# Kernel optimization log

Hardware: AMD Instinct MI355X
Metric: run time of the kernel (lower is better)

Reference implementation:

```python
import jax, jax.numpy as jnp
import numpy as np

N, L, H, D = 4, 2048, 16, 32   # batch, seq len, heads, projection_dim
DIM = H * D                     # 512 model dim


def setup_inputs() -> dict:
    rng = jax.random.key(0)
    k1, k2, k3, k4, k5 = jax.random.split(rng, 5)
    query = jax.random.normal(k1, (N, L, DIM), dtype=jnp.float32)
    key = jax.random.normal(k2, (N, L, DIM), dtype=jnp.float32)
    scale = 0.02
    Wq = jax.random.normal(k3, (DIM, DIM), dtype=jnp.float32) * scale
    Wk = jax.random.normal(k4, (DIM, DIM), dtype=jnp.float32) * scale
    Wv = jax.random.normal(k5, (DIM, DIM), dtype=jnp.float32) * scale
    return {"query": query, "key": key, "Wq": Wq, "Wk": Wk, "Wv": Wv, "mask": 1}


def reference(query, key, Wq, Wk, Wv, mask):
    # torch Linear(bias=False): y = x @ W^T
    n, Lq, _ = query.shape
    _, Lk, _ = key.shape
    q = (query @ Wq.T).reshape(n, Lq, H, D).transpose(0, 2, 1, 3)  # (N,H,Lq,D)
    k = (key @ Wk.T).reshape(n, Lk, H, D).transpose(0, 2, 1, 3)    # (N,H,Lk,D)
    v = (key @ Wv.T).reshape(n, Lk, H, D).transpose(0, 2, 1, 3)    # (N,H,Lk,D)
    q = jax.nn.softmax(q, axis=-1)
    k = jax.nn.softmax(k, axis=-1)
    # causal branch (mask truthy): Lq*Lk > D^2*Lk, so the module takes the
    # cumsum-of-outer-products ("right") path:
    #   right = cumsum_l( k_l outer v_l );  out_l = q_l @ right_l
    kv = jnp.einsum('nhld,nhle->nhlde', k, v)   # (N,H,Lk,D,D) outer products
    S = jnp.cumsum(kv, axis=2)                  # running prefix state
    out = jnp.einsum('nhld,nhlde->nhle', q, S)  # (N,H,Lq,D)
    return out.transpose(0, 2, 1, 3).reshape(n, Lq, H * D)
```

## Files before the change

### kernel.cpp

```cpp
#include <hip/hip_runtime.h>

#define NB      4
#define L_SEQ   2048
#define H_HEADS 16
#define D32     32
#define DIM     512
#define NH      (NB * H_HEADS)
#define CHUNK   64
#define NCHUNK  (L_SEQ / CHUNK)

typedef __attribute__((ext_vector_type(8))) short bf16x8;
typedef __attribute__((ext_vector_type(4))) float f32x4;

__device__ __forceinline__ unsigned short f2bf(float x) {
    unsigned u = __float_as_uint(x);
    u += 0x7fff + ((u >> 16) & 1);
    return (unsigned short)(u >> 16);
}
__device__ __forceinline__ unsigned pack2(float lo, float hi) {
    return (unsigned)f2bf(lo) | ((unsigned)f2bf(hi) << 16);
}

#define QN  4194304
#define WN  262144
#define TOT (2*QN + 3*WN)
__global__ __launch_bounds__(256) void convert_kernel(
    const float* __restrict__ query, const float* __restrict__ key,
    const float* __restrict__ Wq, const float* __restrict__ Wk,
    const float* __restrict__ Wv, unsigned short* __restrict__ dst)
{
    int idx = (blockIdx.x * 256 + threadIdx.x) * 8;
    const float* src; int off;
    if (idx < QN)               { src = query; off = idx; }
    else if (idx < 2*QN)        { src = key;   off = idx - QN; }
    else if (idx < 2*QN + WN)   { src = Wq;    off = idx - 2*QN; }
    else if (idx < 2*QN + 2*WN) { src = Wk;    off = idx - 2*QN - WN; }
    else                        { src = Wv;    off = idx - 2*QN - 2*WN; }
    float4 a = *(const float4*)(src + off);
    float4 b = *(const float4*)(src + off + 4);
    *(uint4*)(dst + idx) = make_uint4(pack2(a.x, a.y), pack2(a.z, a.w),
                                      pack2(b.x, b.y), pack2(b.z, b.w));
}

__global__ __launch_bounds__(256) void gemm3_mfma_kernel(
    const unsigned short* __restrict__ qb, const unsigned short* __restrict__ kb2,
    const unsigned short* __restrict__ wqb, const unsigned short* __restrict__ wkb,
    const unsigned short* __restrict__ wvb,
    unsigned short* __restrict__ Qs, unsigned short* __restrict__ Ks,
    unsigned short* __restrict__ Vt)
{
    const int z  = blockIdx.z;
    const int bx = blockIdx.x >> 6;
    const int by = blockIdx.x & 63;
    const unsigned short *PA, *PB;
    int m0, n0;
    if (z == 0)      { PA = qb;  PB = wqb; m0 = by*128; n0 = bx*128; }
    else if (z == 1) { PA = kb2; PB = wkb; m0 = by*128; n0 = bx*128; }
    else             { PA = wvb; PB = kb2; m0 = bx*128; n0 = by*128; }

    __shared__ unsigned short Asm[128 * 32];
    __shared__ unsigned short Bsm[128 * 32];

    const int t    = threadIdx.x;
    const int w    = t >> 6;
    const int lane = t & 63;
    const int wm   = w >> 1, wn = w & 1;
    const int chunkoff = ((lane & 15) * 4 + (lane >> 4)) * 8;

    f32x4 acc[4][4] = {};

    for (int kb = 0; kb < DIM; kb += 32) {
        #pragma unroll
        for (int rep = 0; rep < 2; rep++) {
            int li  = t + rep * 256;
            int row = li >> 2, kq = li & 3;
            uint4 av = *(const uint4*)(PA + (size_t)(m0 + row) * DIM + kb + kq * 8);
            uint4 bv = *(const uint4*)(PB + (size_t)(n0 + row) * DIM + kb + kq * 8);
            ((uint4*)Asm)[li] = av;
            ((uint4*)Bsm)[li] = bv;
        }
        __syncthreads();

        bf16x8 af[4], bfr[4];
        #pragma unroll
        for (int i = 0; i < 4; i++)
            af[i] = *(const bf16x8*)(Asm + (wm * 4 + i) * 512 + chunkoff);
        #pragma unroll
        for (int j = 0; j < 4; j++)
            bfr[j] = *(const bf16x8*)(Bsm + (wn * 4 + j) * 512 + chunkoff);
        #pragma unroll
        for (int i = 0; i < 4; i++)
            #pragma unroll
            for (int j = 0; j < 4; j++)
                acc[i][j] = __builtin_amdgcn_mfma_f32_16x16x32_bf16(
                    af[i], bfr[j], acc[i][j], 0, 0, 0);
        __syncthreads();
    }

    if (z < 2) {
        #pragma unroll
        for (int i = 0; i < 4; i++)
            #pragma unroll
            for (int jp = 0; jp < 2; jp++)
                #pragma unroll
                for (int r = 0; r < 4; r++) {
                    float a = acc[i][2 * jp][r], b = acc[i][2 * jp + 1][r];
                    float m = fmaxf(a, b);
                    #pragma unroll
                    for (int off = 1; off < 16; off <<= 1)
                        m = fmaxf(m, __shfl_xor(m, off, 64));
                    float ea = __expf(a - m), eb = __expf(b - m);
                    float s = ea + eb;
                    #pragma unroll
                    for (int off = 1; off < 16; off <<= 1)
                        s += __shfl_xor(s, off, 64);
                    float inv = 1.0f / s;
                    acc[i][2 * jp][r]     = ea * inv;
                    acc[i][2 * jp + 1][r] = eb * inv;
                }
    }

    const int quad = lane >> 4, lm = lane & 15;
    #pragma unroll
    for (int i = 0; i < 4; i++) {
        int rbase = m0 + wm * 64 + i * 16 + quad * 4;
        #pragma unroll
        for (int r = 0; r < 4; r++) {
            int rg = rbase + r;
            #pragma unroll
            for (int j = 0; j < 4; j++) {
                int cg = n0 + wn * 64 + j * 16 + lm;
                unsigned short val = f2bf(acc[i][j][r]);
                if (z < 2) {
                    int n = rg >> 11, l = rg & 2047;
                    int h = cg >> 5,  e = cg & 31;
                    unsigned short* dp = (z == 0) ? Qs : Ks;
                    dp[(((size_t)(n * H_HEADS + h)) * L_SEQ + l) * D32 + e] = val;
                } else {
                    int h = rg >> 5,  e = rg & 31;
                    int n = cg >> 11, l = cg & 2047;
                    Vt[(((size_t)(n * H_HEADS + h)) * D32 + e) * L_SEQ + l] = val;
                }
            }
        }
    }
}

__global__ __launch_bounds__(64) void chunk_kv_mfma_kernel(
    const unsigned short* __restrict__ Ks, const unsigned short* __restrict__ Vt,
    float* __restrict__ ckvT)
{
    const int c = blockIdx.x, nh = blockIdx.y;
    const int lane = threadIdx.x;
    const int lm = lane & 15, quad = lane >> 4;

    __shared__ unsigned short Kl[64 * 36];

    {
        const unsigned short* kg = Ks + ((size_t)nh * L_SEQ + c * CHUNK + lane) * D32;
        #pragma unroll
        for (int i = 0; i < 4; i++) {
            uint4 v = *(const uint4*)(kg + i * 8);
            *(uint4*)(Kl + lane * 36 + i * 8) = v;
        }
    }
    __syncthreads();

    f32x4 acc[2][2] = {};
    #pragma unroll
    for (int ch = 0; ch < 2; ch++) {
        bf16x8 aV[2], bK[2];
        #pragma unroll
        for (int mt = 0; mt < 2; mt++)
            aV[mt] = *(const bf16x8*)(Vt + ((size_t)nh * D32 + mt * 16 + lm) * L_SEQ
                                         + c * CHUNK + ch * 32 + quad * 8);
        #pragma unroll
        for (int nt = 0; nt < 2; nt++) {
            const unsigned short* kp = Kl + (ch * 32 + quad * 8) * 36 + nt * 16 + lm;
            #pragma unroll
            for (int j = 0; j < 8; j++) bK[nt][j] = (short)kp[j * 36];
        }
        #pragma unroll
        for (int mt = 0; mt < 2; mt++)
            #pragma unroll
            for (int nt = 0; nt < 2; nt++)
                acc[mt][nt] = __builtin_amdgcn_mfma_f32_16x16x32_bf16(
                    aV[mt], bK[nt], acc[mt][nt], 0, 0, 0);
    }
    #pragma unroll
    for (int mt = 0; mt < 2; mt++)
        #pragma unroll
        for (int nt = 0; nt < 2; nt++)
            #pragma unroll
            for (int r = 0; r < 4; r++) {
                int e = mt * 16 + quad * 4 + r;
                int d = nt * 16 + lm;
                ckvT[(((size_t)nh * NCHUNK + c) * 32 + e) * 32 + d] = acc[mt][nt][r];
            }
}

__global__ __launch_bounds__(64) void prefix_kernel(
    const float* __restrict__ ckvT, unsigned short* __restrict__ SpT)
{
    int nh   = blockIdx.y;
    int slot = blockIdx.x * 64 + threadIdx.x;
    const float* base = ckvT + (size_t)nh * NCHUNK * 1024 + slot * 4;
    unsigned short* sp = SpT + (size_t)nh * NCHUNK * 1024 + slot * 4;
    float4 acc = make_float4(0.f, 0.f, 0.f, 0.f);
    #pragma unroll
    for (int cb = 0; cb < NCHUNK; cb += 8) {
        float4 v[8];
        #pragma unroll
        for (int j = 0; j < 8; j++)
            v[j] = *(const float4*)(base + (size_t)(cb + j) * 1024);
        #pragma unroll
        for (int j = 0; j < 8; j++) {
            ushort4 u;
            u.x = f2bf(acc.x); u.y = f2bf(acc.y);
            u.z = f2bf(acc.z); u.w = f2bf(acc.w);
            *(ushort4*)(sp + (size_t)(cb + j) * 1024) = u;
            acc.x += v[j].x; acc.y += v[j].y;
            acc.z += v[j].z; acc.w += v[j].w;
        }
    }
}

__global__ __launch_bounds__(64) void chunk_out_mfma_kernel(
    const unsigned short* __restrict__ Qs, const unsigned short* __restrict__ Ks,
    const unsigned short* __restrict__ Vt, const unsigned short* __restrict__ SpT,
    float* __restrict__ out)
{
    const int c = blockIdx.x, nh = blockIdx.y;
    __shared__ unsigned short P[64 * 72];

    const int lane = threadIdx.x;
    const int lm = lane & 15, quad = lane >> 4;

    bf16x8 aQ[4], bK[4];
    #pragma unroll
    for (int i = 0; i < 4; i++)
        aQ[i] = *(const bf16x8*)(Qs + ((size_t)nh * L_SEQ + c * CHUNK + i * 16 + lm) * D32
                                    + quad * 8);
    #pragma unroll
    for (int j = 0; j < 4; j++)
        bK[j] = *(const bf16x8*)(Ks + ((size_t)nh * L_SEQ + c * CHUNK + j * 16 + lm) * D32
                                    + quad * 8);

    #pragma unroll
    for (int i = 0; i < 4; i++) {
        #pragma unroll
        for (int j = 0; j < 4; j++) {
            f32x4 p = {};
            if (j <= i) {
                p = __builtin_amdgcn_mfma_f32_16x16x32_bf16(aQ[i], bK[j], p, 0, 0, 0);
                if (j == i) {
                    #pragma unroll
                    for (int r = 0; r < 4; r++)
                        if (lm > quad * 4 + r) p[r] = 0.f;
                }
            }
            #pragma unroll
            for (int r = 0; r < 4; r++)
                P[(i * 16 + quad * 4 + r) * 72 + j * 16 + lm] = f2bf(p[r]);
        }
    }
    __syncthreads();

    bf16x8 bS[2], bV[2][2];
    #pragma unroll
    for (int nt = 0; nt < 2; nt++) {
        bS[nt] = *(const bf16x8*)(SpT + (((size_t)nh * NCHUNK + c) * 32 + nt * 16 + lm) * 32
                                      + quad * 8);
        #pragma unroll
        for (int ch = 0; ch < 2; ch++)
            bV[nt][ch] = *(const bf16x8*)(Vt + ((size_t)nh * D32 + nt * 16 + lm) * L_SEQ
                                             + c * CHUNK + ch * 32 + quad * 8);
    }

    const int n = nh >> 4, h = nh & 15;
    #pragma unroll
    for (int i = 0; i < 4; i++) {
        const int chmax = (i >> 1) + 1;
        bf16x8 aP[2];
        for (int ch = 0; ch < chmax; ch++)
            aP[ch] = *(const bf16x8*)&P[(i * 16 + lm) * 72 + ch * 32 + quad * 8];
        #pragma unroll
        for (int nt = 0; nt < 2; nt++) {
            f32x4 acc = {};
            acc = __builtin_amdgcn_mfma_f32_16x16x32_bf16(aQ[i], bS[nt], acc, 0, 0, 0);
            for (int ch = 0; ch < chmax; ch++)
                acc = __builtin_amdgcn_mfma_f32_16x16x32_bf16(aP[ch], bV[nt][ch], acc, 0, 0, 0);
            #pragma unroll
            for (int r = 0; r < 4; r++) {
                int lg = c * CHUNK + i * 16 + quad * 4 + r;
                out[((size_t)n * L_SEQ + lg) * DIM + h * D32 + nt * 16 + lm] = acc[r];
            }
        }
    }
}

extern "C" void kernel_launch(void* const* d_in, const int* in_sizes, int n_in,
                              void* d_out, int out_size, void* d_ws, size_t ws_size,
                              hipStream_t stream)
{
    (void)in_sizes; (void)n_in; (void)out_size; (void)ws_size;
    const float* query = (const float*)d_in[0];
    const float* key   = (const float*)d_in[1];
    const float* Wq    = (const float*)d_in[2];
    const float* Wk    = (const float*)d_in[3];
    const float* Wv    = (const float*)d_in[4];
    float* out = (float*)d_out;

    unsigned short* bf = (unsigned short*)d_ws;
    unsigned short* qb  = bf;
    unsigned short* kb  = qb + QN;
    unsigned short* wqb = kb + QN;
    unsigned short* wkb = wqb + WN;
    unsigned short* wvb = wkb + WN;
    unsigned short* Qs  = wvb + WN;
    const size_t SZ = (size_t)NH * L_SEQ * D32;
    unsigned short* Ks  = Qs + SZ;
    unsigned short* Vt  = Ks + SZ;
    unsigned short* SpT = Vt + SZ;
    float* ckvT = (float*)(SpT + (size_t)NH * NCHUNK * 1024);

    convert_kernel<<<dim3(TOT / (256 * 8)), dim3(256), 0, stream>>>(
        query, key, Wq, Wk, Wv, qb);
    gemm3_mfma_kernel<<<dim3(256, 1, 3), dim3(256), 0, stream>>>(
        qb, kb, wqb, wkb, wvb, Qs, Ks, Vt);
    chunk_kv_mfma_kernel<<<dim3(NCHUNK, NH), dim3(64), 0, stream>>>(Ks, Vt, ckvT);
    prefix_kernel<<<dim3(4, NH), dim3(64), 0, stream>>>(ckvT, SpT);
    chunk_out_mfma_kernel<<<dim3(NCHUNK, NH), dim3(64), 0, stream>>>(Qs, Ks, Vt, SpT, out);
}
```

Before: 140.9 us.

## Double-buffer GEMM LDS tiles with direct global-to-LDS loads and XOR swizzle

The projection GEMM's operand tiles now go straight from global memory into LDS through global_load_lds, into two buffers, so the next K-slice is fetched while MFMAs run on the current one. LDS placement uses an XOR swizzle on the 16-byte chunks to reduce bank conflicts on the fragment reads, and one barrier per step is removed. This doubles LDS use per block and relies on the barrier to order the asynchronous LDS writes against the reads.

```diff
diff --git a/kernel.cpp b/kernel.cpp
--- a/kernel.cpp
+++ b/kernel.cpp
@@ -42,6 +42,10 @@
                                       pack2(b.x, b.y), pack2(b.z, b.w));
 }
 
+#define GLL(g, l) __builtin_amdgcn_global_load_lds( \
+    (const __attribute__((address_space(1))) unsigned int*)(g), \
+    (__attribute__((address_space(3))) unsigned int*)(l), 16, 0, 0)
+
 __global__ __launch_bounds__(256) void gemm3_mfma_kernel(
     const unsigned short* __restrict__ qb, const unsigned short* __restrict__ kb2,
     const unsigned short* __restrict__ wqb, const unsigned short* __restrict__ wkb,
@@ -58,44 +62,62 @@
     else if (z == 1) { PA = kb2; PB = wkb; m0 = by*128; n0 = bx*128; }
     else             { PA = wvb; PB = kb2; m0 = bx*128; n0 = by*128; }
 
-    __shared__ unsigned short Asm[128 * 32];
-    __shared__ unsigned short Bsm[128 * 32];
+    __shared__ unsigned short Asm[2 * 4096];
+    __shared__ unsigned short Bsm[2 * 4096];
 
     const int t    = threadIdx.x;
     const int w    = t >> 6;
     const int lane = t & 63;
     const int wm   = w >> 1, wn = w & 1;
-    const int chunkoff = ((lane & 15) * 4 + (lane >> 4)) * 8;
+    const int lm   = lane & 15, quad = lane >> 4;
+
+    const int qswz = quad ^ ((lm >> 1) & 3);
+    const int aoff = (wm * 64 + lm) * 32 + qswz * 8;
+    const int boff = (wn * 64 + lm) * 32 + qswz * 8;
+
+    const int li0 = t, li1 = t + 256;
+    const int row0 = li0 >> 2, row1 = li1 >> 2;
+    const int qs0 = (li0 & 3) ^ ((li0 >> 3) & 3);
+    const int qs1 = (li1 & 3) ^ ((li1 >> 3) & 3);
+    const unsigned short* gA0 = PA + (size_t)(m0 + row0) * DIM + qs0 * 8;
+    const unsigned short* gA1 = PA + (size_t)(m0 + row1) * DIM + qs1 * 8;
+    const unsigned short* gB0 = PB + (size_t)(n0 + row0) * DIM + qs0 * 8;
+    const unsigned short* gB1 = PB + (size_t)(n0 + row1) * DIM + qs1 * 8;
 
     f32x4 acc[4][4] = {};
 
-    for (int kb = 0; kb < DIM; kb += 32) {
-        #pragma unroll
-        for (int rep = 0; rep < 2; rep++) {
-            int li  = t + rep * 256;
-            int row = li >> 2, kq = li & 3;
-            uint4 av = *(const uint4*)(PA + (size_t)(m0 + row) * DIM + kb + kq * 8);
-            uint4 bv = *(const uint4*)(PB + (size_t)(n0 + row) * DIM + kb + kq * 8);
-            ((uint4*)Asm)[li] = av;
-            ((uint4*)Bsm)[li] = bv;
-        }
-        __syncthreads();
-
+#define STAGE(buf, kb) do { \
+    GLL(gA0 + (kb), Asm + (buf) * 4096 + li0 * 8); \
+    GLL(gB0 + (kb), Bsm + (buf) * 4096 + li0 * 8); \
+    GLL(gA1 + (kb), Asm + (buf) * 4096 + li1 * 8); \
+    GLL(gB1 + (kb), Bsm + (buf) * 4096 + li1 * 8); \
+} while (0)
+
+    STAGE(0, 0);
+    __syncthreads();
+
+    #pragma unroll
+    for (int step = 0; step < 16; ++step) {
+        const int cur = step & 1;
+        if (step < 15) STAGE(cur ^ 1, (step + 1) * 32);
+        const unsigned short* As = Asm + cur * 4096;
+        const unsigned short* Bs = Bsm + cur * 4096;
         bf16x8 af[4], bfr[4];
         #pragma unroll
         for (int i = 0; i < 4; i++)
-            af[i] = *(const bf16x8*)(Asm + (wm * 4 + i) * 512 + chunkoff);
+            af[i] = *(const bf16x8*)(As + aoff + i * 512);
         #pragma unroll
         for (int j = 0; j < 4; j++)
-            bfr[j] = *(const bf16x8*)(Bsm + (wn * 4 + j) * 512 + chunkoff);
+            bfr[j] = *(const bf16x8*)(Bs + boff + j * 512);
         #pragma unroll
         for (int i = 0; i < 4; i++)
             #pragma unroll
             for (int j = 0; j < 4; j++)
                 acc[i][j] = __builtin_amdgcn_mfma_f32_16x16x32_bf16(
                     af[i], bfr[j], acc[i][j], 0, 0, 0);
-        __syncthreads();
-    }
+        if (step < 15) __syncthreads();
+    }
+#undef STAGE
 
     if (z < 2) {
         #pragma unroll
@@ -120,7 +142,6 @@
                 }
     }
 
-    const int quad = lane >> 4, lm = lane & 15;
     #pragma unroll
     for (int i = 0; i < 4; i++) {
         int rbase = m0 + wm * 64 + i * 16 + quad * 4;
```

After: 141.6 us. About the same (+0.5%).
